# Performance work log

Hardware: AMD Instinct MI355X
Metric: run time of the kernel (lower is better)

Reference implementation:

```python
import jax, jax.numpy as jnp
import numpy as np

N_ENT, N_USR, N_ITEM, N_REL, N_CLS, N_FAC, D = 100000, 4096, 8192, 32, 3, 8, 128
N_EDGES, NNZ = 800000, 204800


def setup_inputs() -> dict:
    key = jax.random.key(0)
    ks = jax.random.split(key, 15)
    return {
        "entity_emb": jax.random.normal(ks[0], (N_ENT, D), jnp.float32),
        "item_emb": jax.random.normal(ks[1], (N_ITEM, D), jnp.float32),
        "user_emb": jax.random.normal(ks[2], (N_USR, D), jnp.float32),
        "latent_emb": jax.random.normal(ks[3], (N_FAC, D), jnp.float32),
        "relation_emb": jax.random.normal(ks[4], (N_REL, D), jnp.float32),
        "edge_index": jax.random.randint(ks[5], (2, N_EDGES), 0, N_ENT, jnp.int32),
        "edge_type": jax.random.randint(ks[6], (N_EDGES,), 0, N_REL, jnp.int32),
        "edge_imp": jax.random.uniform(ks[7], (N_EDGES,), jnp.float32),
        "inter_rows": jax.random.randint(ks[8], (NNZ,), 0, N_USR, jnp.int32),
        "inter_cols": jax.random.randint(ks[9], (NNZ,), 0, N_ENT, jnp.int32),
        "inter_vals": jax.random.uniform(ks[10], (NNZ,), jnp.float32),
        "disen_weight_att": jax.random.normal(ks[11], (N_FAC, N_REL), jnp.float32),
        "ent_rel_w": jax.random.normal(ks[12], (N_REL, D), jnp.float32),
        "usr_cls_w": jax.random.normal(ks[13], (N_CLS, D), jnp.float32),
        "inter_cls_mat": jax.random.normal(ks[14], (N_CLS, N_USR, N_ITEM), jnp.float32),
    }


def reference(entity_emb, item_emb, user_emb, latent_emb, relation_emb,
              edge_index, edge_type, edge_imp, inter_rows, inter_cols,
              inter_vals, disen_weight_att, ent_rel_w, usr_cls_w, inter_cls_mat):
    n_entities = entity_emb.shape[0]
    n_users = user_emb.shape[0]
    head, tail = edge_index[0], edge_index[1]

    # --- entity aggregation, e_mode='att_imp' ---
    # per-entity attention over relations: [n_ent, n_rel]
    ent_rel_att = jax.nn.softmax(entity_emb @ relation_emb.T, axis=1)
    mess_att = ent_rel_att[head, edge_type][:, None]              # [E,1]
    message_score = relation_emb[edge_type] * mess_att * edge_imp[:, None]  # [E,D]
    message = entity_emb[tail] * message_score                    # [E,D]
    entity_agg = jax.ops.segment_sum(message, head, num_segments=n_entities)

    # --- user aggregation, u_mode='inter_cls' ---
    # sparse interact_mat @ entity_emb via COO gather + segment_sum
    user_agg = jax.ops.segment_sum(entity_emb[inter_cols] * inter_vals[:, None],
                                   inter_rows, num_segments=n_users)
    user_cls_att = jax.nn.softmax(user_emb @ usr_cls_w.T, axis=1)  # [U,C]
    item_emb_2 = item_emb * relation_emb.sum(axis=0, keepdims=True)  # [I,D]
    # stack_c(inter_cls_mat[c] @ item_emb_2).transpose(0,1) -> [U,C,D]
    disen_weight = jnp.einsum('cui,id->ucd', inter_cls_mat, item_emb_2)
    user_agg = user_agg + (disen_weight * user_cls_att[:, :, None]).sum(axis=1)

    return entity_agg, user_agg
```

## Files before the change

kernel.cpp:

```cpp
#include <hip/hip_runtime.h>

#define N_ENT   100000
#define N_USR   4096
#define N_ITEM  8192
#define N_REL   32
#define N_CLS   3
#define DD      128
#define N_EDGES 800000
#define NNZ     204800

#define CAP_E   64
#define CAP_U   128

typedef __attribute__((ext_vector_type(8))) short short8;
typedef __attribute__((ext_vector_type(4))) short short4v;
typedef __attribute__((ext_vector_type(4))) float f32x4;

static __device__ __forceinline__ unsigned short f2bf(float x) {
    unsigned int u = __builtin_bit_cast(unsigned int, x);
    u = (u + 0x7fffu + ((u >> 16) & 1u)) >> 16;
    return (unsigned short)u;
}
static __device__ __forceinline__ float bflo(unsigned int v) {
    return __uint_as_float(v << 16);
}
static __device__ __forceinline__ float bfhi(unsigned int v) {
    return __uint_as_float(v & 0xffff0000u);
}

#define ZB  ((N_ENT + N_USR + 255) / 256)

__global__ __launch_bounds__(256) void k_prep_light(const float* __restrict__ rel,
                                                    int* __restrict__ cnt,
                                                    const float* __restrict__ item,
                                                    unsigned short* __restrict__ Bt,
                                                    const float* __restrict__ usr,
                                                    const float* __restrict__ w,
                                                    float* __restrict__ uatt) {
    __shared__ float smem[32 * 33 + 32];
    int bx = blockIdx.x;

    if (bx < ZB) {
        int i = bx * 256 + threadIdx.x;
        if (i < N_ENT + N_USR) cnt[i] = 0;
        return;
    }
    bx -= ZB;

    if (bx < 1024) {
        float (*tile)[33] = (float(*)[33])smem;
        float* ssum = smem + 32 * 33;
        const int b2 = bx & 255, by = bx >> 8;
        const int tx = threadIdx.x & 31, ty = threadIdx.x >> 5;
        const int i0 = b2 * 32, d0 = by * 32;
        if (threadIdx.x < 32) {
            float s = 0.f;
            for (int r = 0; r < N_REL; ++r) s += rel[r * DD + d0 + threadIdx.x];
            ssum[threadIdx.x] = s;
        }
#pragma unroll
        for (int rr = 0; rr < 4; ++rr)
            tile[ty + 8 * rr][tx] = item[(size_t)(i0 + ty + 8 * rr) * DD + d0 + tx];
        __syncthreads();
#pragma unroll
        for (int rr = 0; rr < 4; ++rr) {
            int d = d0 + ty + 8 * rr;
            Bt[(size_t)d * N_ITEM + i0 + tx] = f2bf(tile[tx][ty + 8 * rr] * ssum[ty + 8 * rr]);
        }
        return;
    }
    bx -= 1024;

    {
        for (int i = threadIdx.x; i < N_CLS * DD; i += 256) smem[i] = w[i];
        __syncthreads();
        int u = bx * 256 + threadIdx.x;
        const float4* row = (const float4*)(usr + (size_t)u * DD);
        float acc[3] = {0.f, 0.f, 0.f};
        for (int dq = 0; dq < DD / 4; ++dq) {
            float4 v = row[dq];
#pragma unroll
            for (int c = 0; c < 3; ++c) {
                float4 ww = *(const float4*)&smem[c * DD + dq * 4];
                acc[c] += v.x * ww.x + v.y * ww.y + v.z * ww.z + v.w * ww.w;
            }
        }
        float m = fmaxf(acc[0], fmaxf(acc[1], acc[2]));
        float s = 0.f;
#pragma unroll
        for (int c = 0; c < 3; ++c) { acc[c] = __expf(acc[c] - m); s += acc[c]; }
        float inv = 1.f / s;
#pragma unroll
        for (int c = 0; c < 3; ++c) uatt[u * 3 + c] = acc[c] * inv;
    }
}

#define PLANE  ((long long)N_USR * N_ITEM)
#define PLANE4 (PLANE / 4)
#define CB_BLOCKS ((int)(PLANE / 4096))
#define EAB ((N_ENT + 255) / 256)
#define SCAT_BLOCKS ((N_EDGES + 255) / 256)

__global__ __launch_bounds__(256) void k_node2(const float* __restrict__ icm,
                                               const float* __restrict__ uatt,
                                               unsigned short* __restrict__ Abf,
                                               const float* __restrict__ ent,
                                               const float* __restrict__ rel,
                                               float* __restrict__ att,
                                               unsigned short* __restrict__ entbf,
                                               unsigned short* __restrict__ relbf,
                                               const int* __restrict__ eidx,
                                               const int* __restrict__ etyp,
                                               const float* __restrict__ eimp,
                                               const int* __restrict__ irow,
                                               const int* __restrict__ icol,
                                               const float* __restrict__ ival,
                                               int* __restrict__ cnt,
                                               int2* __restrict__ pack_e,
                                               int2* __restrict__ pack_u) {
    __shared__ float smemf[N_REL * DD];

    if (blockIdx.x < CB_BLOCKS) {
        const int bid = blockIdx.x;
        const int u = bid >> 1;
        const float a0 = uatt[u * 3 + 0];
        const float a1 = uatt[u * 3 + 1];
        const float a2 = uatt[u * 3 + 2];
        const float4* icm4 = (const float4*)icm;
        const long long base4 = (long long)bid * 1024 + threadIdx.x;
#pragma unroll
        for (int j = 0; j < 4; ++j) {
            long long idx4 = base4 + j * 256;
            float4 f0 = icm4[idx4];
            float4 f1 = icm4[idx4 + PLANE4];
            float4 f2 = icm4[idx4 + 2 * PLANE4];
            ushort4 o;
            o.x = f2bf(a0 * f0.x + a1 * f1.x + a2 * f2.x);
            o.y = f2bf(a0 * f0.y + a1 * f1.y + a2 * f2.y);
            o.z = f2bf(a0 * f0.z + a1 * f1.z + a2 * f2.z);
            o.w = f2bf(a0 * f0.w + a1 * f1.w + a2 * f2.w);
            ((ushort4*)Abf)[idx4] = o;
        }
        return;
    }

    if (blockIdx.x < CB_BLOCKS + EAB) {
        int bx = blockIdx.x - CB_BLOCKS;
        for (int i = threadIdx.x; i < N_REL * DD; i += 256) smemf[i] = rel[i];
        __syncthreads();
        if (bx == 0) {
            for (int i = threadIdx.x; i < N_REL * DD; i += 256)
                relbf[i] = f2bf(smemf[i]);
        }
        int e = bx * 256 + threadIdx.x;
        if (e >= N_ENT) return;
        const float4* row = (const float4*)(ent + (size_t)e * DD);
        unsigned short* brow = entbf + (size_t)e * DD;
        float acc[N_REL];
#pragma unroll
        for (int r = 0; r < N_REL; ++r) acc[r] = 0.f;
        for (int dq = 0; dq < DD / 4; ++dq) {
            float4 v = row[dq];
            ushort4 bv;
            bv.x = f2bf(v.x); bv.y = f2bf(v.y); bv.z = f2bf(v.z); bv.w = f2bf(v.w);
            *(ushort4*)(brow + dq * 4) = bv;
#pragma unroll
            for (int r = 0; r < N_REL; ++r) {
                float4 ww = *(const float4*)&smemf[r * DD + dq * 4];
                acc[r] += v.x * ww.x + v.y * ww.y + v.z * ww.z + v.w * ww.w;
            }
        }
        float m = acc[0];
#pragma unroll
        for (int r = 1; r < N_REL; ++r) m = fmaxf(m, acc[r]);
        float s = 0.f;
#pragma unroll
        for (int r = 0; r < N_REL; ++r) { acc[r] = __expf(acc[r] - m); s += acc[r]; }
        float inv = 1.f / s;
        float* o = att + (size_t)e * N_REL;
#pragma unroll
        for (int r = 0; r < N_REL; ++r) o[r] = acc[r] * inv;
        return;
    }

    {
        int i = (blockIdx.x - CB_BLOCKS - EAB) * 256 + threadIdx.x;
        if (i < N_EDGES) {
            int h = eidx[i], tl = eidx[N_EDGES + i], r = etyp[i];
            int p = atomicAdd(&cnt[h], 1);
            if (p < CAP_E) {
                int2 pk;
                pk.x = tl | (r << 24);
                pk.y = __float_as_int(eimp[i]);
                pack_e[(size_t)h * CAP_E + p] = pk;
            }
        }
        if (i < NNZ) {
            int u = irow[i];
            int p = atomicAdd(&cnt[N_ENT + u], 1);
            if (p < CAP_U) {
                int2 pk;
                pk.x = icol[i];
                pk.y = __float_as_int(ival[i]);
                pack_u[(size_t)u * CAP_U + p] = pk;
            }
        }
    }
}

#define BM 64
#define BK 32
#define SPLITK 16
#define KCH (N_ITEM / SPLITK)
#define NSTEP (KCH / BK)

__global__ __launch_bounds__(256) void k_gemm2(const unsigned short* __restrict__ Abf,
                                               const unsigned short* __restrict__ Bt,
                                               float* __restrict__ part) {
    __shared__ unsigned short sA[BM][40];
    __shared__ unsigned short sB[DD][40];

    const int t  = threadIdx.x;
    const int m0 = blockIdx.x * BM;
    const long long k0b = (long long)blockIdx.y * KCH;

    const int ua = t >> 3;
    const int qa = t & 7;
    const int db = t >> 2;
    const int qb = t & 3;

    const int lane = t & 63;
    const int wv = t >> 6;
    const int wm = wv >> 1, wn = wv & 1;
    const int la = lane & 15, lb = lane >> 4;

    f32x4 acc[2][4];
#pragma unroll
    for (int mi = 0; mi < 2; ++mi)
#pragma unroll
        for (int ni = 0; ni < 4; ++ni) {
            f32x4 z = {0.f, 0.f, 0.f, 0.f};
            acc[mi][ni] = z;
        }

    short4v rA0, rA1;
    short8 rB0, rB1;

#define GISSUE(step) do {                                                     \
    const long long k0_ = k0b + (long long)(step) * BK;                       \
    rA0 = *(const short4v*)(Abf + (size_t)(m0 + ua) * N_ITEM + k0_ + qa * 4); \
    rA1 = *(const short4v*)(Abf + (size_t)(m0 + ua + 32) * N_ITEM + k0_ + qa * 4); \
    rB0 = *(const short8*)(Bt + (size_t)db * N_ITEM + k0_ + qb * 8);          \
    rB1 = *(const short8*)(Bt + (size_t)(db + 64) * N_ITEM + k0_ + qb * 8);   \
} while (0)

    GISSUE(0);

#pragma unroll 1
    for (int s = 0; s < NSTEP; ++s) {
        __syncthreads();
        *(short4v*)(&sA[ua][qa * 4]) = rA0;
        *(short4v*)(&sA[ua + 32][qa * 4]) = rA1;
        *(short8*)(&sB[db][qb * 8]) = rB0;
        *(short8*)(&sB[db + 64][qb * 8]) = rB1;
        __syncthreads();
        if (s + 1 < NSTEP) GISSUE(s + 1);

        short8 af[2], bfr[4];
#pragma unroll
        for (int mi = 0; mi < 2; ++mi)
            af[mi] = *(const short8*)(&sA[wm * 32 + mi * 16 + la][0] + lb * 8);
#pragma unroll
        for (int ni = 0; ni < 4; ++ni)
            bfr[ni] = *(const short8*)(&sB[wn * 64 + ni * 16 + la][0] + lb * 8);
#pragma unroll
        for (int mi = 0; mi < 2; ++mi)
#pragma unroll
            for (int ni = 0; ni < 4; ++ni)
                acc[mi][ni] = __builtin_amdgcn_mfma_f32_16x16x32_bf16(
                    af[mi], bfr[ni], acc[mi][ni], 0, 0, 0);
    }
#undef GISSUE

    float* pbase = part + (size_t)blockIdx.y * ((size_t)N_USR * DD);
#pragma unroll
    for (int mi = 0; mi < 2; ++mi)
#pragma unroll
        for (int ni = 0; ni < 4; ++ni)
#pragma unroll
            for (int r = 0; r < 4; ++r) {
                int row = m0 + wm * 32 + mi * 16 + lb * 4 + r;
                int col = wn * 64 + ni * 16 + la;
                pbase[(size_t)row * DD + col] = acc[mi][ni][r];
            }
}

#define EDGE_BLOCKS (N_ENT / 16)
#define USER_BLOCKS (N_USR / 4)

__global__ __launch_bounds__(256) void k_node3(const unsigned short* __restrict__ entbf,
                                               const unsigned short* __restrict__ relbf,
                                               const float* __restrict__ att,
                                               const int2* __restrict__ pack_e,
                                               const int2* __restrict__ pack_u,
                                               const int* __restrict__ cnt,
                                               const float* __restrict__ part,
                                               float* __restrict__ out_ent,
                                               float* __restrict__ out_usr) {
    const int lane = threadIdx.x & 63;

    if (blockIdx.x < EDGE_BLOCKS) {
        const int wid = blockIdx.x * 4 + (threadIdx.x >> 6);
        const int l15 = lane & 15;
        const int grp = lane >> 4;
#pragma unroll 1
        for (int hh = 0; hh < 4; ++hh) {
            const int h = wid * 4 + hh;
            const int n = min(cnt[h], CAP_E);
            const float attv = att[(size_t)h * N_REL + (lane & 31)];
            const int2* seg = pack_e + (size_t)h * CAP_E;
            float acc[8];
#pragma unroll
            for (int e = 0; e < 8; ++e) acc[e] = 0.f;
            for (int j = 0; j < n; j += 8) {
                const int e0 = j + grp, e1 = j + 4 + grp;
                int2 p0 = seg[min(e0, n - 1)];
                int2 p1 = seg[min(e1, n - 1)];
                const int r0 = ((unsigned)p0.x) >> 24;
                const int r1 = ((unsigned)p1.x) >> 24;
                float s0 = __shfl(attv, r0, 64) * __int_as_float(p0.y);
                float s1 = __shfl(attv, r1, 64) * __int_as_float(p1.y);
                s0 = (e0 < n) ? s0 : 0.f;
                s1 = (e1 < n) ? s1 : 0.f;
                uint4 b0 = ((const uint4*)(entbf + (size_t)(p0.x & 0xFFFFFF) * DD))[l15];
                uint4 b1 = ((const uint4*)(entbf + (size_t)(p1.x & 0xFFFFFF) * DD))[l15];
                uint4 v0 = ((const uint4*)(relbf + (size_t)r0 * DD))[l15];
                uint4 v1 = ((const uint4*)(relbf + (size_t)r1 * DD))[l15];
                const unsigned* bp0 = (const unsigned*)&b0;
                const unsigned* bp1 = (const unsigned*)&b1;
                const unsigned* vp0 = (const unsigned*)&v0;
                const unsigned* vp1 = (const unsigned*)&v1;
#pragma unroll
                for (int q = 0; q < 4; ++q) {
                    acc[2 * q]     = fmaf(bflo(bp0[q]) * bflo(vp0[q]), s0, acc[2 * q]);
                    acc[2 * q + 1] = fmaf(bfhi(bp0[q]) * bfhi(vp0[q]), s0, acc[2 * q + 1]);
                    acc[2 * q]     = fmaf(bflo(bp1[q]) * bflo(vp1[q]), s1, acc[2 * q]);
                    acc[2 * q + 1] = fmaf(bfhi(bp1[q]) * bfhi(vp1[q]), s1, acc[2 * q + 1]);
                }
            }
#pragma unroll
            for (int e = 0; e < 8; ++e) {
                acc[e] += __shfl_xor(acc[e], 16, 64);
                acc[e] += __shfl_xor(acc[e], 32, 64);
            }
            if (lane < 16) {
                float4 o0 = {acc[0], acc[1], acc[2], acc[3]};
                float4 o1 = {acc[4], acc[5], acc[6], acc[7]};
                float4* dst = (float4*)(out_ent + (size_t)h * DD) + l15 * 2;
                dst[0] = o0;
                dst[1] = o1;
            }
        }
    } else {
        const int u = (blockIdx.x - EDGE_BLOCKS) * 4 + (threadIdx.x >> 6);
        const int n = min(cnt[N_ENT + u], CAP_U);
        const int2* seg = pack_u + (size_t)u * CAP_U;
        float ax = 0.f, ay = 0.f;
        for (int j = 0; j < n; j += 8) {
            int2 pk[8];
#pragma unroll
            for (int k = 0; k < 8; ++k) pk[k] = seg[min(j + k, n - 1)];
            unsigned int bv[8];
            float sc[8];
#pragma unroll
            for (int k = 0; k < 8; ++k) {
                sc[k] = (j + k < n) ? __int_as_float(pk[k].y) : 0.f;
                bv[k] = ((const unsigned int*)(entbf + (size_t)pk[k].x * DD))[lane];
            }
#pragma unroll
            for (int k = 0; k < 8; ++k) {
                ax = fmaf(bflo(bv[k]), sc[k], ax);
                ay = fmaf(bfhi(bv[k]), sc[k], ay);
            }
        }
#pragma unroll
        for (int k = 0; k < SPLITK; ++k) {
            float2 p = ((const float2*)(part + (size_t)k * N_USR * DD + (size_t)u * DD))[lane];
            ax += p.x;
            ay += p.y;
        }
        float2 o; o.x = ax; o.y = ay;
        ((float2*)(out_usr + (size_t)u * DD))[lane] = o;
    }
}

static constexpr size_t algn(size_t x) { return (x + 255) & ~(size_t)255; }

extern "C" void kernel_launch(void* const* d_in, const int* in_sizes, int n_in,
                              void* d_out, int out_size, void* d_ws, size_t ws_size,
                              hipStream_t stream) {
    const float* ent  = (const float*)d_in[0];
    const float* item = (const float*)d_in[1];
    const float* usr  = (const float*)d_in[2];
    const float* rel  = (const float*)d_in[4];
    const int*   eidx = (const int*)d_in[5];
    const int*   etyp = (const int*)d_in[6];
    const float* eimp = (const float*)d_in[7];
    const int*   irow = (const int*)d_in[8];
    const int*   icol = (const int*)d_in[9];
    const float* ival = (const float*)d_in[10];
    const float* uclw = (const float*)d_in[13];
    const float* icm  = (const float*)d_in[14];

    float* out_ent = (float*)d_out;
    float* out_usr = out_ent + (size_t)N_ENT * DD;

    char* w = (char*)d_ws;
    size_t o = 0;
    float* ws_att  = (float*)(w + o);  o = algn(o + (size_t)N_ENT * N_REL * 4);
    float* ws_uatt = (float*)(w + o);  o = algn(o + (size_t)N_USR * N_CLS * 4);
    unsigned short* ws_Bt    = (unsigned short*)(w + o); o = algn(o + (size_t)DD * N_ITEM * 2);
    unsigned short* ws_entbf = (unsigned short*)(w + o); o = algn(o + (size_t)N_ENT * DD * 2);
    unsigned short* ws_relbf = (unsigned short*)(w + o); o = algn(o + (size_t)N_REL * DD * 2);
    unsigned short* ws_Abf   = (unsigned short*)(w + o); o = algn(o + (size_t)N_USR * N_ITEM * 2);
    int*  ws_cnt   = (int*)(w + o);  o = algn(o + (size_t)(N_ENT + N_USR) * 4);
    int2* pack_e   = (int2*)(w + o); o = algn(o + (size_t)N_ENT * CAP_E * 8);
    int2* pack_u   = (int2*)(w + o); o = algn(o + (size_t)N_USR * CAP_U * 8);
    float* part    = (float*)(w + o); o = algn(o + (size_t)SPLITK * N_USR * DD * 4);

    (void)in_sizes; (void)n_in; (void)ws_size; (void)out_size;

    k_prep_light<<<ZB + 1024 + 16, 256, 0, stream>>>(rel, ws_cnt, item, ws_Bt,
                                                     usr, uclw, ws_uatt);
    k_node2<<<CB_BLOCKS + EAB + SCAT_BLOCKS, 256, 0, stream>>>(
        icm, ws_uatt, ws_Abf, ent, rel, ws_att, ws_entbf, ws_relbf,
        eidx, etyp, eimp, irow, icol, ival, ws_cnt, pack_e, pack_u);
    k_gemm2<<<dim3(N_USR / BM, SPLITK), 256, 0, stream>>>(ws_Abf, ws_Bt, part);
    k_node3<<<EDGE_BLOCKS + USER_BLOCKS, 256, 0, stream>>>(ws_entbf, ws_relbf, ws_att,
                                                           pack_e, pack_u, ws_cnt, part,
                                                           out_ent, out_usr);
}
```

Baseline: 299.3 us.

## Split node kernel into prep, grid-stride combine, and scatter launches

Moves the entity attention/bf16 conversion into the first prep kernel and splits the former multi-role node kernel into a grid-stride class-combine kernel (2048 blocks) and a separate edge/interaction scatter kernel. This is meant to stop the heavy 32-relation attention blocks and the atomic scatter blocks from sharing a launch with the bandwidth-bound combine, and to cut block-launch overhead for the streaming combine. The cost is an extra kernel launch and serialisation between phases that previously overlapped within one grid.

New measurement: 335.6 us. 1.12x slower.

```diff
diff --git a/kernel.cpp b/kernel.cpp
--- a/kernel.cpp
+++ b/kernel.cpp
@@ -28,24 +28,61 @@
     return __uint_as_float(v & 0xffff0000u);
 }
 
+#define EAB ((N_ENT + 255) / 256)
 #define ZB  ((N_ENT + N_USR + 255) / 256)
 
-__global__ __launch_bounds__(256) void k_prep_light(const float* __restrict__ rel,
-                                                    int* __restrict__ cnt,
-                                                    const float* __restrict__ item,
-                                                    unsigned short* __restrict__ Bt,
-                                                    const float* __restrict__ usr,
-                                                    const float* __restrict__ w,
-                                                    float* __restrict__ uatt) {
-    __shared__ float smem[32 * 33 + 32];
+__global__ __launch_bounds__(256) void k_prep_full(const float* __restrict__ ent,
+                                                   const float* __restrict__ rel,
+                                                   float* __restrict__ att,
+                                                   unsigned short* __restrict__ entbf,
+                                                   unsigned short* __restrict__ relbf,
+                                                   int* __restrict__ cnt,
+                                                   const float* __restrict__ item,
+                                                   unsigned short* __restrict__ Bt,
+                                                   const float* __restrict__ usr,
+                                                   const float* __restrict__ w,
+                                                   float* __restrict__ uatt) {
+    __shared__ float smem[N_REL * DD];
     int bx = blockIdx.x;
 
-    if (bx < ZB) {
-        int i = bx * 256 + threadIdx.x;
-        if (i < N_ENT + N_USR) cnt[i] = 0;
+    if (bx < EAB) {
+        for (int i = threadIdx.x; i < N_REL * DD; i += 256) smem[i] = rel[i];
+        __syncthreads();
+        if (bx == 0) {
+            for (int i = threadIdx.x; i < N_REL * DD; i += 256)
+                relbf[i] = f2bf(smem[i]);
+        }
+        int e = bx * 256 + threadIdx.x;
+        if (e >= N_ENT) return;
+        const float4* row = (const float4*)(ent + (size_t)e * DD);
+        unsigned short* brow = entbf + (size_t)e * DD;
+        float acc[N_REL];
+#pragma unroll
+        for (int r = 0; r < N_REL; ++r) acc[r] = 0.f;
+        for (int dq = 0; dq < DD / 4; ++dq) {
+            float4 v = row[dq];
+            ushort4 bv;
+            bv.x = f2bf(v.x); bv.y = f2bf(v.y); bv.z = f2bf(v.z); bv.w = f2bf(v.w);
+            *(ushort4*)(brow + dq * 4) = bv;
+#pragma unroll
+            for (int r = 0; r < N_REL; ++r) {
+                float4 ww = *(const float4*)&smem[r * DD + dq * 4];
+                acc[r] += v.x * ww.x + v.y * ww.y + v.z * ww.z + v.w * ww.w;
+            }
+        }
+        float m = acc[0];
+#pragma unroll
+        for (int r = 1; r < N_REL; ++r) m = fmaxf(m, acc[r]);
+        float s = 0.f;
+#pragma unroll
+        for (int r = 0; r < N_REL; ++r) { acc[r] = __expf(acc[r] - m); s += acc[r]; }
+        float inv = 1.f / s;
+        float* o = att + (size_t)e * N_REL;
+#pragma unroll
+        for (int r = 0; r < N_REL; ++r) o[r] = acc[r] * inv;
         return;
     }
-    bx -= ZB;
+    bx -= EAB;
 
     if (bx < 1024) {
         float (*tile)[33] = (float(*)[33])smem;
@@ -71,6 +108,13 @@
     }
     bx -= 1024;
 
+    if (bx < ZB) {
+        int i = bx * 256 + threadIdx.x;
+        if (i < N_ENT + N_USR) cnt[i] = 0;
+        return;
+    }
+    bx -= ZB;
+
     {
         for (int i = threadIdx.x; i < N_CLS * DD; i += 256) smem[i] = w[i];
         __syncthreads();
@@ -97,113 +141,61 @@
 
 #define PLANE  ((long long)N_USR * N_ITEM)
 #define PLANE4 (PLANE / 4)
-#define CB_BLOCKS ((int)(PLANE / 4096))
-#define EAB ((N_ENT + 255) / 256)
-#define SCAT_BLOCKS ((N_EDGES + 255) / 256)
-
-__global__ __launch_bounds__(256) void k_node2(const float* __restrict__ icm,
-                                               const float* __restrict__ uatt,
-                                               unsigned short* __restrict__ Abf,
-                                               const float* __restrict__ ent,
-                                               const float* __restrict__ rel,
-                                               float* __restrict__ att,
-                                               unsigned short* __restrict__ entbf,
-                                               unsigned short* __restrict__ relbf,
-                                               const int* __restrict__ eidx,
-                                               const int* __restrict__ etyp,
-                                               const float* __restrict__ eimp,
-                                               const int* __restrict__ irow,
-                                               const int* __restrict__ icol,
-                                               const float* __restrict__ ival,
-                                               int* __restrict__ cnt,
-                                               int2* __restrict__ pack_e,
-                                               int2* __restrict__ pack_u) {
-    __shared__ float smemf[N_REL * DD];
-
-    if (blockIdx.x < CB_BLOCKS) {
-        const int bid = blockIdx.x;
-        const int u = bid >> 1;
+
+__global__ __launch_bounds__(256) void k_combine(const float* __restrict__ icm,
+                                                 const float* __restrict__ uatt,
+                                                 unsigned short* __restrict__ Abf) {
+    const float4* icm4 = (const float4*)icm;
+    ushort4* out4 = (ushort4*)Abf;
+    long long idx = (long long)blockIdx.x * 256 + threadIdx.x;
+    const long long stride = (long long)gridDim.x * 256;
+    for (; idx < PLANE4; idx += stride) {
+        const int u = (int)(idx >> 11);
         const float a0 = uatt[u * 3 + 0];
         const float a1 = uatt[u * 3 + 1];
         const float a2 = uatt[u * 3 + 2];
-        const float4* icm4 = (const float4*)icm;
-        const long long base4 = (long long)bid * 1024 + threadIdx.x;
-#pragma unroll
-        for (int j = 0; j < 4; ++j) {
-            long long idx4 = base4 + j * 256;
-            float4 f0 = icm4[idx4];
-            float4 f1 = icm4[idx4 + PLANE4];
-            float4 f2 = icm4[idx4 + 2 * PLANE4];
-            ushort4 o;
-            o.x = f2bf(a0 * f0.x + a1 * f1.x + a2 * f2.x);
-            o.y = f2bf(a0 * f0.y + a1 * f1.y + a2 * f2.y);
-            o.z = f2bf(a0 * f0.z + a1 * f1.z + a2 * f2.z);
-            o.w = f2bf(a0 * f0.w + a1 * f1.w + a2 * f2.w);
-            ((ushort4*)Abf)[idx4] = o;
-        }
-        return;
-    }
-
-    if (blockIdx.x < CB_BLOCKS + EAB) {
-        int bx = blockIdx.x - CB_BLOCKS;
-        for (int i = threadIdx.x; i < N_REL * DD; i += 256) smemf[i] = rel[i];
-        __syncthreads();
-        if (bx == 0) {
-            for (int i = threadIdx.x; i < N_REL * DD; i += 256)
-                relbf[i] = f2bf(smemf[i]);
-        }
-        int e = bx * 256 + threadIdx.x;
-        if (e >= N_ENT) return;
-        const float4* row = (const float4*)(ent + (size_t)e * DD);
-        unsigned short* brow = entbf + (size_t)e * DD;
-        float acc[N_REL];
-#pragma unroll
-        for (int r = 0; r < N_REL; ++r) acc[r] = 0.f;
-        for (int dq = 0; dq < DD / 4; ++dq) {
-            float4 v = row[dq];
-            ushort4 bv;
-            bv.x = f2bf(v.x); bv.y = f2bf(v.y); bv.z = f2bf(v.z); bv.w = f2bf(v.w);
-            *(ushort4*)(brow + dq * 4) = bv;
-#pragma unroll
-            for (int r = 0; r < N_REL; ++r) {
-                float4 ww = *(const float4*)&smemf[r * DD + dq * 4];
-                acc[r] += v.x * ww.x + v.y * ww.y + v.z * ww.z + v.w * ww.w;
-            }
-        }
-        float m = acc[0];
-#pragma unroll
-        for (int r = 1; r < N_REL; ++r) m = fmaxf(m, acc[r]);
-        float s = 0.f;
-#pragma unroll
-        for (int r = 0; r < N_REL; ++r) { acc[r] = __expf(acc[r] - m); s += acc[r]; }
-        float inv = 1.f / s;
-        float* o = att + (size_t)e * N_REL;
-#pragma unroll
-        for (int r = 0; r < N_REL; ++r) o[r] = acc[r] * inv;
-        return;
-    }
-
-    {
-        int i = (blockIdx.x - CB_BLOCKS - EAB) * 256 + threadIdx.x;
-        if (i < N_EDGES) {
-            int h = eidx[i], tl = eidx[N_EDGES + i], r = etyp[i];
-            int p = atomicAdd(&cnt[h], 1);
-            if (p < CAP_E) {
-                int2 pk;
-                pk.x = tl | (r << 24);
-                pk.y = __float_as_int(eimp[i]);
-                pack_e[(size_t)h * CAP_E + p] = pk;
-            }
-        }
-        if (i < NNZ) {
-            int u = irow[i];
-            int p = atomicAdd(&cnt[N_ENT + u], 1);
-            if (p < CAP_U) {
-                int2 pk;
-                pk.x = icol[i];
-                pk.y = __float_as_int(ival[i]);
-                pack_u[(size_t)u * CAP_U + p] = pk;
-            }
+        float4 f0 = icm4[idx];
+        float4 f1 = icm4[idx + PLANE4];
+        float4 f2 = icm4[idx + 2 * PLANE4];
+        ushort4 o;
+        o.x = f2bf(a0 * f0.x + a1 * f1.x + a2 * f2.x);
+        o.y = f2bf(a0 * f0.y + a1 * f1.y + a2 * f2.y);
+        o.z = f2bf(a0 * f0.z + a1 * f1.z + a2 * f2.z);
+        o.w = f2bf(a0 * f0.w + a1 * f1.w + a2 * f2.w);
+        out4[idx] = o;
+    }
+}
+
+#define SCAT_BLOCKS ((N_EDGES + 255) / 256)
+
+__global__ __launch_bounds__(256) void k_scatter(const int* __restrict__ eidx,
+                                                 const int* __restrict__ etyp,
+                                                 const float* __restrict__ eimp,
+                                                 const int* __restrict__ irow,
+                                                 const int* __restrict__ icol,
+                                                 const float* __restrict__ ival,
+                                                 int* __restrict__ cnt,
+                                                 int2* __restrict__ pack_e,
+                                                 int2* __restrict__ pack_u) {
+    int i = blockIdx.x * 256 + threadIdx.x;
+    if (i < N_EDGES) {
+        int h = eidx[i], tl = eidx[N_EDGES + i], r = etyp[i];
+        int p = atomicAdd(&cnt[h], 1);
+        if (p < CAP_E) {
+            int2 pk;
+            pk.x = tl | (r << 24);
+            pk.y = __float_as_int(eimp[i]);
+            pack_e[(size_t)h * CAP_E + p] = pk;
+        }
+    }
+    if (i < NNZ) {
+        int u = irow[i];
+        int p = atomicAdd(&cnt[N_ENT + u], 1);
+        if (p < CAP_U) {
+            int2 pk;
+            pk.x = icol[i];
+            pk.y = __float_as_int(ival[i]);
+            pack_u[(size_t)u * CAP_U + p] = pk;
         }
     }
 }
@@ -430,11 +422,12 @@
 
     (void)in_sizes; (void)n_in; (void)ws_size; (void)out_size;
 
-    k_prep_light<<<ZB + 1024 + 16, 256, 0, stream>>>(rel, ws_cnt, item, ws_Bt,
-                                                     usr, uclw, ws_uatt);
-    k_node2<<<CB_BLOCKS + EAB + SCAT_BLOCKS, 256, 0, stream>>>(
-        icm, ws_uatt, ws_Abf, ent, rel, ws_att, ws_entbf, ws_relbf,
-        eidx, etyp, eimp, irow, icol, ival, ws_cnt, pack_e, pack_u);
+    k_prep_full<<<EAB + 1024 + ZB + 16, 256, 0, stream>>>(ent, rel, ws_att, ws_entbf,
+                                                          ws_relbf, ws_cnt, item, ws_Bt,
+                                                          usr, uclw, ws_uatt);
+    k_combine<<<2048, 256, 0, stream>>>(icm, ws_uatt, ws_Abf);
+    k_scatter<<<SCAT_BLOCKS, 256, 0, stream>>>(eidx, etyp, eimp, irow, icol, ival,
+                                               ws_cnt, pack_e, pack_u);
     k_gemm2<<<dim3(N_USR / BM, SPLITK), 256, 0, stream>>>(ws_Abf, ws_Bt, part);
     k_node3<<<EDGE_BLOCKS + USER_BLOCKS, 256, 0, stream>>>(ws_entbf, ws_relbf, ws_att,
                                                            pack_e, pack_u, ws_cnt, part,
```
